# Kernel optimization log

Measured on AMD Instinct MI355X. Metric: run time of the kernel, lower is better.

The kernel has to match this reference:

```python
import jax, jax.numpy as jnp
import numpy as np

N, E, R = 50000, 1600000, 8
IN_F, HID_F, OUT_F = 128, 64, 64


def setup_inputs() -> dict:
    key = jax.random.key(0)
    ks = jax.random.split(key, 9)
    x = jax.random.normal(ks[0], (N, IN_F), dtype=jnp.float32)
    edge_index = jax.random.randint(ks[1], (2, E), 0, N, dtype=jnp.int64)
    edge_type = jax.random.randint(ks[2], (E,), 0, R, dtype=jnp.int64)
    # layer 1 params (scaled like glorot)
    s1 = 1.0 / np.sqrt(IN_F)
    W1_rel = jax.random.normal(ks[3], (R, IN_F, HID_F), dtype=jnp.float32) * s1
    W1_root = jax.random.normal(ks[4], (IN_F, HID_F), dtype=jnp.float32) * s1
    b1 = jnp.zeros((HID_F,), dtype=jnp.float32)
    # layer 2 params
    s2 = 1.0 / np.sqrt(HID_F)
    W2_rel = jax.random.normal(ks[5], (R, HID_F, OUT_F), dtype=jnp.float32) * s2
    W2_root = jax.random.normal(ks[6], (HID_F, OUT_F), dtype=jnp.float32) * s2
    b2 = jnp.zeros((OUT_F,), dtype=jnp.float32)
    return {"x": x, "edge_index": edge_index, "edge_type": edge_type,
            "W1_rel": W1_rel, "W1_root": W1_root, "b1": b1,
            "W2_rel": W2_rel, "W2_root": W2_root, "b2": b2}


def _rgcn_conv(x, src, dst, etype, W_rel, W_root, b):
    """PyG RGCNConv: root transform + per-relation mean-aggregated messages."""
    n = x.shape[0]
    r = W_rel.shape[0]
    # per-relation transform of all node features: [R, N, H]
    xw = jnp.einsum('nd,rdh->rnh', x, W_rel)
    # per-edge message: transformed source feature under the edge's relation
    msg = xw[etype, src]  # [E, H]
    # mean normalization per (dst, relation) pair
    key = dst * r + etype  # [E]
    cnt = jax.ops.segment_sum(jnp.ones(etype.shape, dtype=x.dtype), key,
                              num_segments=n * r)
    inv = 1.0 / jnp.maximum(cnt, 1.0)
    msg = msg * inv[key][:, None]
    # scatter-add into target nodes
    agg = jax.ops.segment_sum(msg, dst, num_segments=n)  # [N, H]
    return agg + x @ W_root + b


def reference(x, edge_index, edge_type, W1_rel, W1_root, b1, W2_rel, W2_root, b2):
    src, dst = edge_index[0], edge_index[1]
    h = _rgcn_conv(x, src, dst, edge_type, W1_rel, W1_root, b1)
    h = jax.nn.relu(h)
    out = _rgcn_conv(h, src, dst, edge_type, W2_rel, W2_root, b2)
    return out
```

## Files before the change

### kernel.cpp

```cpp
#include <hip/hip_runtime.h>


constexpr int NN  = 50000;
constexpr int NE  = 1600000;
constexpr int NR  = 8;
constexpr int FIN = 128;
constexpr int FH  = 64;

constexpr int BSH = 7;
constexpr int BN  = 1 << BSH;
constexpr int NB  = (NN + BN - 1) >> BSH;
constexpr int CAP = 6144;
constexpr int CH  = 4096;
constexpr int NAPP = (NE + CH - 1) / CH;
constexpr unsigned XWMAX = (unsigned)(NN - 1) * (NR * 64) + (NR - 1) * 64;

typedef __attribute__((ext_vector_type(8))) short bf16x8;
typedef __attribute__((ext_vector_type(4))) float f32x4;

__device__ __forceinline__ unsigned short f2bf(float f) {
  unsigned u = __float_as_uint(f);
  u = (u + 0x7fff + ((u >> 16) & 1)) >> 16;
  return (unsigned short)u;
}
__device__ __forceinline__ float bf2f(unsigned short b) {
  return __uint_as_float(((unsigned)b) << 16);
}
__device__ __forceinline__ bool edge_ok(unsigned s, unsigned d, unsigned r) {
  return s < NN && d < NN && r < NR;
}

__device__ void append_body(char* smem, int bx,
                            const int* __restrict__ src,
                            const int* __restrict__ dst,
                            const int* __restrict__ et,
                            int* __restrict__ bcur,
                            unsigned* __restrict__ brecs) {
  uint2* stage = (uint2*)smem;
  int* h     = (int*)(smem + (size_t)CH * 8);
  int* gbase = h + NB;
  int* sbase = gbase + NB;
  int* scur  = sbase + NB;
  int* wtot  = scur + NB;

  const int t  = threadIdx.x;
  const int c0 = bx * CH;
  const int m  = min(CH, NE - c0);

  for (int i = t; i < NB; i += 256) h[i] = 0;
  __syncthreads();

  for (int i = t; i < m; i += 256) {
    const unsigned s = (unsigned)src[c0 + i];
    const unsigned d = (unsigned)dst[c0 + i];
    const unsigned r = (unsigned)et[c0 + i];
    if (edge_ok(s, d, r)) atomicAdd(&h[d >> BSH], 1);
  }
  __syncthreads();

  const int v0 = (2 * t < NB) ? h[2 * t] : 0;
  const int v1 = (2 * t + 1 < NB) ? h[2 * t + 1] : 0;
  if (2 * t < NB     && v0) gbase[2 * t]     = atomicAdd(&bcur[2 * t], v0);
  if (2 * t + 1 < NB && v1) gbase[2 * t + 1] = atomicAdd(&bcur[2 * t + 1], v1);
  const int s = v0 + v1;
  int incl = s;
#pragma unroll
  for (int o = 1; o < 64; o <<= 1) {
    int u = __shfl_up(incl, o, 64);
    if ((t & 63) >= o) incl += u;
  }
  if ((t & 63) == 63) wtot[t >> 6] = incl;
  __syncthreads();
  int wo = 0;
  for (int w = 0; w < (t >> 6); ++w) wo += wtot[w];
  const int e = wo + incl - s;
  if (2 * t < NB)     { sbase[2 * t] = e;          scur[2 * t] = e; }
  if (2 * t + 1 < NB) { sbase[2 * t + 1] = e + v0; scur[2 * t + 1] = e + v0; }
  __syncthreads();

  for (int i = t; i < m; i += 256) {
    const unsigned sv = (unsigned)src[c0 + i];
    const unsigned d  = (unsigned)dst[c0 + i];
    const unsigned r  = (unsigned)et[c0 + i];
    if (edge_ok(sv, d, r)) {
      const int p = atomicAdd(&scur[d >> BSH], 1);
      if (p < CH) stage[p] = make_uint2((sv << 10) | (((unsigned)d & (BN - 1)) << 3) | r, d);
    }
  }
  __syncthreads();

  const int M = min(sbase[NB - 1] + h[NB - 1], CH);
  for (int j = t; j < M; j += 256) {
    const uint2 rec = stage[j];
    const int b = (int)(rec.y >> BSH);
    const int idx = min(gbase[b] + (j - sbase[b]), NB * CAP - 1);
    brecs[idx] = rec.x;
  }
}

__global__ void __launch_bounds__(256) bucket_finalize(
    const int* __restrict__ bcur, const unsigned* __restrict__ brecs,
    int* __restrict__ row_start, int* __restrict__ deg,
    unsigned* __restrict__ recs) {
  const int b    = blockIdx.x;
  const int base = b * CAP;
  const int m    = min(bcur[b] - base, CAP);
  const int d0   = b << BSH;
  __shared__ int cnt[BN * NR];
  __shared__ int curs[BN * NR];
  __shared__ int wtot[4];
  const int t = threadIdx.x;

  for (int i = t; i < BN * NR; i += 256) cnt[i] = 0;
  __syncthreads();
  for (int i = t; i < m; i += 256) {
    const unsigned rec = brecs[base + i];
    const int dl = (int)((rec >> 3) & (BN - 1));
    const int r  = (int)(rec & 7);
    atomicAdd(&cnt[dl * NR + r], 1);
  }
  __syncthreads();

  const int c0 = cnt[t * 4], c1 = cnt[t * 4 + 1], c2 = cnt[t * 4 + 2], c3 = cnt[t * 4 + 3];
  const int s = c0 + c1 + c2 + c3;
  int incl = s;
#pragma unroll
  for (int o = 1; o < 64; o <<= 1) {
    int u = __shfl_up(incl, o, 64);
    if ((t & 63) >= o) incl += u;
  }
  if ((t & 63) == 63) wtot[t >> 6] = incl;
  __syncthreads();
  int wo = 0;
  for (int w = 0; w < (t >> 6); ++w) wo += wtot[w];
  const int e = wo + incl - s;
  curs[t * 4]     = e;
  curs[t * 4 + 1] = e + c0;
  curs[t * 4 + 2] = e + c0 + c1;
  curs[t * 4 + 3] = e + c0 + c1 + c2;
  __syncthreads();

  if (t < BN) {
    const int d = d0 + t;
    if (d < NN) {
      const int start = curs[t * NR];
      const int end   = (t == BN - 1) ? m : curs[(t + 1) * NR];
      row_start[d] = base + start;
      deg[d]       = end - start;
    }
  }
  __syncthreads();

  for (int i = t; i < m; i += 256) {
    const unsigned rec = brecs[base + i];
    const int dl = (int)((rec >> 3) & (BN - 1));
    const int r  = (int)(rec & 7);
    const unsigned sv = rec >> 10;
    const int p  = atomicAdd(&curs[dl * NR + r], 1);
    const unsigned cn = (unsigned)min(cnt[dl * NR + r], 127);
    recs[base + min(p, CAP - 1)] = (cn << 25) | (sv << 9) | ((unsigned)r << 6);
  }
}

__global__ void prep(const float* __restrict__ W1r, const float* __restrict__ W1o,
                     const float* __restrict__ W2r, const float* __restrict__ W2o,
                     unsigned short* __restrict__ Wt1,
                     unsigned short* __restrict__ Wt2,
                     int* __restrict__ bcur) {
  const int i  = blockIdx.x * blockDim.x + threadIdx.x;
  if (i < NB) bcur[i] = i * CAP;
  const int n1 = (NR + 1) * 64 * FIN;
  const int n2 = (NR + 1) * 64 * FH;
  if (i < n1) {
    const int g = i / (64 * FIN), rem = i % (64 * FIN);
    const int n = rem / FIN, k = rem % FIN;
    const float* W = (g < NR) ? (W1r + (size_t)g * FIN * 64) : W1o;
    Wt1[i] = f2bf(W[k * 64 + n]);
  } else if (i < n1 + n2) {
    const int j = i - n1;
    const int g = j / (64 * FH), rem = j % (64 * FH);
    const int n = rem / FH, k = rem % FH;
    const float* W = (g < NR) ? (W2r + (size_t)g * FH * 64) : W2o;
    Wt2[j] = f2bf(W[k * 64 + n]);
  }
}

template <int K, bool A_FP32>
__device__ void gemm_body(char* smem, int bx,
                          const void* __restrict__ Av,
                          const unsigned short* __restrict__ Wt,
                          const float* __restrict__ bias,
                          unsigned short* __restrict__ xw,
                          float* __restrict__ root_out) {
  constexpr int KP  = K + 8;
  constexpr int NCH = 64 * (K / 8) / 256;
  constexpr int NKC = K / 32;
  unsigned short* Bs0 = (unsigned short*)smem;
  const int n0  = bx * 64;
  const int tid = threadIdx.x;
  const int wave = tid >> 6, lane = tid & 63;
  const int i16 = lane & 15, quad = lane >> 4;
  const int r0 = wave * 16 + i16;
  const int arow = n0 + r0;

  bf16x8 afrag[NKC];
  if constexpr (A_FP32) {
    const float* A = (const float*)Av;
#pragma unroll
    for (int kc = 0; kc < NKC; ++kc) {
      bf16x8 v = {};
      if (arow < NN) {
        const float* p = A + (size_t)arow * K + kc * 32 + quad * 8;
        const float4 f0 = *(const float4*)p;
        const float4 f1 = *(const float4*)(p + 4);
        v[0] = f2bf(f0.x); v[1] = f2bf(f0.y); v[2] = f2bf(f0.z); v[3] = f2bf(f0.w);
        v[4] = f2bf(f1.x); v[5] = f2bf(f1.y); v[6] = f2bf(f1.z); v[7] = f2bf(f1.w);
      }
      afrag[kc] = v;
    }
  } else {
    const unsigned short* A = (const unsigned short*)Av;
#pragma unroll
    for (int kc = 0; kc < NKC; ++kc) {
      bf16x8 v = {};
      if (arow < NN) v = *(const bf16x8*)(A + (size_t)arow * K + kc * 32 + quad * 8);
      afrag[kc] = v;
    }
  }

  for (int c = 0; c < NCH; ++c) {
    const int idx = tid + c * 256;
    const int row = idx / (K / 8), kp = (idx % (K / 8)) * 8;
    *(bf16x8*)(Bs0 + row * KP + kp) = *(const bf16x8*)(Wt + idx * 8);
  }
  __syncthreads();

  for (int g = 0; g <= NR; ++g) {
    const int buf = g & 1;
    unsigned short* Bc = Bs0 + buf * 64 * KP;
    unsigned short* Bn = Bs0 + (buf ^ 1) * 64 * KP;
    bf16x8 breg[NCH];
    if (g < NR) {
      const unsigned short* Wn = Wt + (size_t)(g + 1) * 64 * K;
#pragma unroll
      for (int c = 0; c < NCH; ++c) breg[c] = *(const bf16x8*)(Wn + (tid + c * 256) * 8);
    }

    f32x4 acc[4] = {};
#pragma unroll
    for (int kc = 0; kc < NKC; ++kc) {
      const int k0 = kc * 32 + quad * 8;
      const bf16x8 a0 = afrag[kc];
      const bf16x8 b0 = *(const bf16x8*)(Bc + (i16)      * KP + k0);
      const bf16x8 b1 = *(const bf16x8*)(Bc + (i16 + 16) * KP + k0);
      const bf16x8 b2 = *(const bf16x8*)(Bc + (i16 + 32) * KP + k0);
      const bf16x8 b3 = *(const bf16x8*)(Bc + (i16 + 48) * KP + k0);
      acc[0] = __builtin_amdgcn_mfma_f32_16x16x32_bf16(a0, b0, acc[0], 0, 0, 0);
      acc[1] = __builtin_amdgcn_mfma_f32_16x16x32_bf16(a0, b1, acc[1], 0, 0, 0);
      acc[2] = __builtin_amdgcn_mfma_f32_16x16x32_bf16(a0, b2, acc[2], 0, 0, 0);
      acc[3] = __builtin_amdgcn_mfma_f32_16x16x32_bf16(a0, b3, acc[3], 0, 0, 0);
    }

    if (g < NR) {
#pragma unroll
      for (int c = 0; c < NCH; ++c) {
        const int idx = tid + c * 256;
        const int row = idx / (K / 8), kp = (idx % (K / 8)) * 8;
        *(bf16x8*)(Bn + row * KP + kp) = breg[c];
      }
#pragma unroll
      for (int reg = 0; reg < 4; ++reg) {
        const int n = n0 + wave * 16 + quad * 4 + reg;
        if (n >= NN) continue;
        unsigned short* p = xw + (size_t)n * (NR * 64) + g * 64 + i16;
#pragma unroll
        for (int ct = 0; ct < 4; ++ct) p[ct * 16] = f2bf(acc[ct][reg]);
      }
    } else {
      float bv[4];
#pragma unroll
      for (int ct = 0; ct < 4; ++ct) bv[ct] = bias[ct * 16 + i16];
#pragma unroll
      for (int reg = 0; reg < 4; ++reg) {
        const int n = n0 + wave * 16 + quad * 4 + reg;
        if (n >= NN) continue;
        float* p = root_out + (size_t)n * 64 + i16;
#pragma unroll
        for (int ct = 0; ct < 4; ++ct) p[ct * 16] = acc[ct][reg] + bv[ct];
      }
    }
    __syncthreads();
  }
}

__global__ void __launch_bounds__(256) fused_append_gemm1(
    const int* __restrict__ src, const int* __restrict__ dst,
    const int* __restrict__ et, int* __restrict__ bcur,
    unsigned* __restrict__ brecs,
    const float* __restrict__ A, const unsigned short* __restrict__ Wt,
    const float* __restrict__ bias, unsigned short* __restrict__ xw,
    float* __restrict__ root_out) {
  extern __shared__ char smem[];
  const int bx = (int)blockIdx.x;
  if (bx % 3 == 2 && bx / 3 < NAPP)
    append_body(smem, bx / 3, src, dst, et, bcur, brecs);
  else
    gemm_body<FIN, true>(smem, bx - (bx + 1) / 3, A, Wt, bias, xw, root_out);
}

__global__ void __launch_bounds__(256) gemm_l2(
    const unsigned short* __restrict__ A, const unsigned short* __restrict__ Wt,
    const float* __restrict__ bias, unsigned short* __restrict__ xw,
    float* __restrict__ out) {
  extern __shared__ char smem[];
  gemm_body<FH, false>(smem, (int)blockIdx.x, A, Wt, bias, xw, out);
}

template <bool RELU_BF16>
__global__ void __launch_bounds__(256) agg_csr(
    const int* __restrict__ row_start, const int* __restrict__ deg,
    const unsigned* __restrict__ recs, const unsigned short* __restrict__ xw,
    const float* __restrict__ root,
    float* __restrict__ out_f32, unsigned short* __restrict__ out_b16) {
  const int gid  = blockIdx.x * blockDim.x + threadIdx.x;
  const int lane = gid & 63;
  const int wv   = gid >> 6;
  const int half = lane >> 5;
  const int sub  = lane & 31;
  const int e  = sub >> 3;
  const int l8 = sub & 7;
  const int d  = wv * 2 + half;
  if (d >= NN) return;
  const int base = row_start[d];
  const int n    = deg[d];
  const unsigned* po = recs + base;
  const unsigned short* xp = xw + l8 * 8;
  float a[8] = {};

  for (int i0 = 0; i0 < n; i0 += 32) {
    unsigned rr[8];
#pragma unroll
    for (int sl = 0; sl < 8; ++sl) {
      const int i = i0 + e + 4 * sl;
      rr[sl] = (i < n) ? po[i] : 0u;
    }
    bf16x8 vv[8];
#pragma unroll
    for (int sl = 0; sl < 8; ++sl) {
      const unsigned u = min(rr[sl] & 0x01FFFFFFu, XWMAX);
      vv[sl] = *(const bf16x8*)(xp + u);
    }
#pragma unroll
    for (int sl = 0; sl < 8; ++sl) {
      float w = __builtin_amdgcn_rcpf((float)(rr[sl] >> 25));
      if (i0 + e + 4 * sl >= n) w = 0.f;
#pragma unroll
      for (int q = 0; q < 8; ++q) a[q] += bf2f((unsigned short)vv[sl][q]) * w;
    }
  }

#pragma unroll
  for (int q = 0; q < 8; ++q) {
    a[q] += __shfl_xor(a[q], 8, 64);
    a[q] += __shfl_xor(a[q], 16, 64);
  }

  if (e == 0) {
    const float4 r0 = *(const float4*)(root + (size_t)d * 64 + l8 * 8);
    const float4 r1 = *(const float4*)(root + (size_t)d * 64 + l8 * 8 + 4);
    const float o[8] = {r0.x + a[0], r0.y + a[1], r0.z + a[2], r0.w + a[3],
                        r1.x + a[4], r1.y + a[5], r1.z + a[6], r1.w + a[7]};
    if (RELU_BF16) {
      bf16x8 ov;
#pragma unroll
      for (int q = 0; q < 8; ++q) ov[q] = (short)f2bf(fmaxf(o[q], 0.f));
      *(bf16x8*)(out_b16 + (size_t)d * 64 + l8 * 8) = ov;
    } else {
      *(float4*)(out_f32 + (size_t)d * 64 + l8 * 8)     = make_float4(o[0], o[1], o[2], o[3]);
      *(float4*)(out_f32 + (size_t)d * 64 + l8 * 8 + 4) = make_float4(o[4], o[5], o[6], o[7]);
    }
  }
}

extern "C" void kernel_launch(void* const* d_in, const int* in_sizes, int n_in,
                              void* d_out, int out_size, void* d_ws, size_t ws_size,
                              hipStream_t stream) {
  const float* x   = (const float*)d_in[0];
  const int*   ei  = (const int*)d_in[1];
  const int*   et  = (const int*)d_in[2];
  const float* W1r = (const float*)d_in[3];
  const float* W1o = (const float*)d_in[4];
  const float* b1  = (const float*)d_in[5];
  const float* W2r = (const float*)d_in[6];
  const float* W2o = (const float*)d_in[7];
  const float* b2  = (const float*)d_in[8];
  float* out = (float*)d_out;

  const int* src = ei;
  const int* dst = ei + NE;

  char* ws = (char*)d_ws;
  size_t off = 0;
  auto alloc = [&](size_t bytes) {
    void* p = ws + off; off += (bytes + 255) & ~(size_t)255; return p;
  };
  int*   bcur      = (int*)alloc((size_t)NB * 4);
  int*   row_start = (int*)alloc((size_t)NN * 4);
  int*   deg       = (int*)alloc((size_t)NN * 4);
  unsigned* brecs  = (unsigned*)alloc((size_t)NB * CAP * 4);
  unsigned* offs   = (unsigned*)alloc((size_t)NB * CAP * 4);
  unsigned short* xw    = (unsigned short*)alloc((size_t)NN * NR * 64 * 2);
  unsigned short* hb    = (unsigned short*)alloc((size_t)NN * FH * 2);
  float*          hroot = (float*)alloc((size_t)NN * 64 * 4);
  unsigned short* Wt1   = (unsigned short*)alloc((size_t)(NR + 1) * 64 * FIN * 2);
  unsigned short* Wt2   = (unsigned short*)alloc((size_t)(NR + 1) * 64 * FH * 2);

  const int nprep = (NR + 1) * 64 * (FIN + FH);
  prep<<<(nprep + 255) / 256, 256, 0, stream>>>(W1r, W1o, W2r, W2o, Wt1, Wt2, bcur);

  const int gemm_blocks = (NN + 63) / 64;
  const int agg_blocks  = ((NN + 1) / 2 + 3) / 4;
  constexpr int SM1 = CH * 8 + 4 * NB * 4 + 16;
  constexpr int SM2 = 2 * 64 * (FH + 8) * 2;

  fused_append_gemm1<<<NAPP + gemm_blocks, 256, SM1, stream>>>(
      src, dst, et, bcur, brecs, x, Wt1, b1, xw, hroot);
  bucket_finalize<<<NB, 256, 0, stream>>>(bcur, brecs, row_start, deg, offs);

  agg_csr<true><<<agg_blocks, 256, 0, stream>>>(row_start, deg, offs, xw, hroot, nullptr, hb);
  gemm_l2<<<gemm_blocks, 256, SM2, stream>>>(hb, Wt2, b2, xw, out);
  agg_csr<false><<<agg_blocks, 256, 0, stream>>>(row_start, deg, offs, xw, out, out, nullptr);
}
```

Measured before the change: 244.1 us.

## Reorder layer-2 as aggregate-then-transform with a single concatenated-K GEMM

```diff
diff --git a/kernel.cpp b/kernel.cpp
--- a/kernel.cpp
+++ b/kernel.cpp
@@ -14,6 +14,8 @@
 constexpr int CH  = 4096;
 constexpr int NAPP = (NE + CH - 1) / CH;
 constexpr unsigned XWMAX = (unsigned)(NN - 1) * (NR * 64) + (NR - 1) * 64;
+constexpr int K2  = 576;
+constexpr int K2P = 584;
 
 typedef __attribute__((ext_vector_type(8))) short bf16x8;
 typedef __attribute__((ext_vector_type(4))) float f32x4;
@@ -101,7 +103,7 @@
 __global__ void __launch_bounds__(256) bucket_finalize(
     const int* __restrict__ bcur, const unsigned* __restrict__ brecs,
     int* __restrict__ row_start, int* __restrict__ deg,
-    unsigned* __restrict__ recs) {
+    unsigned* __restrict__ recs, unsigned* __restrict__ segs) {
   const int b    = blockIdx.x;
   const int base = b * CAP;
   const int m    = min(bcur[b] - base, CAP);
@@ -147,6 +149,12 @@
       const int end   = (t == BN - 1) ? m : curs[(t + 1) * NR];
       row_start[d] = base + start;
       deg[d]       = end - start;
+#pragma unroll
+      for (int r = 0; r < NR; ++r) {
+        const unsigned st = (unsigned)(base + curs[t * NR + r]);
+        const unsigned cn = (unsigned)min(cnt[t * NR + r], 255);
+        segs[(size_t)d * NR + r] = (st << 8) | cn;
+      }
     }
   }
   __syncthreads();
@@ -165,12 +173,12 @@
 __global__ void prep(const float* __restrict__ W1r, const float* __restrict__ W1o,
                      const float* __restrict__ W2r, const float* __restrict__ W2o,
                      unsigned short* __restrict__ Wt1,
-                     unsigned short* __restrict__ Wt2,
+                     unsigned short* __restrict__ Wt2b,
                      int* __restrict__ bcur) {
   const int i  = blockIdx.x * blockDim.x + threadIdx.x;
   if (i < NB) bcur[i] = i * CAP;
   const int n1 = (NR + 1) * 64 * FIN;
-  const int n2 = (NR + 1) * 64 * FH;
+  const int n2 = 64 * K2;
   if (i < n1) {
     const int g = i / (64 * FIN), rem = i % (64 * FIN);
     const int n = rem / FIN, k = rem % FIN;
@@ -178,10 +186,16 @@
     Wt1[i] = f2bf(W[k * 64 + n]);
   } else if (i < n1 + n2) {
     const int j = i - n1;
-    const int g = j / (64 * FH), rem = j % (64 * FH);
-    const int n = rem / FH, k = rem % FH;
-    const float* W = (g < NR) ? (W2r + (size_t)g * FH * 64) : W2o;
-    Wt2[j] = f2bf(W[k * 64 + n]);
+    const int n = j / K2, c = j % K2;
+    float v;
+    if (c < 512) {
+      const int r = c >> 6, kk = c & 63;
+      v = W2r[((size_t)r * 64 + kk) * 64 + n];
+    } else {
+      const int kk = c - 512;
+      v = W2o[(size_t)kk * 64 + n];
+    }
+    Wt2b[j] = f2bf(v);
   }
 }
 
@@ -308,40 +322,28 @@
     gemm_body<FIN, true>(smem, bx - (bx + 1) / 3, A, Wt, bias, xw, root_out);
 }
 
-__global__ void __launch_bounds__(256) gemm_l2(
-    const unsigned short* __restrict__ A, const unsigned short* __restrict__ Wt,
-    const float* __restrict__ bias, unsigned short* __restrict__ xw,
-    float* __restrict__ out) {
-  extern __shared__ char smem[];
-  gemm_body<FH, false>(smem, (int)blockIdx.x, A, Wt, bias, xw, out);
-}
-
-template <bool RELU_BF16>
-__global__ void __launch_bounds__(256) agg_csr(
+__global__ void __launch_bounds__(256) agg1(
     const int* __restrict__ row_start, const int* __restrict__ deg,
     const unsigned* __restrict__ recs, const unsigned short* __restrict__ xw,
-    const float* __restrict__ root,
-    float* __restrict__ out_f32, unsigned short* __restrict__ out_b16) {
+    const float* __restrict__ root, unsigned short* __restrict__ out_b16) {
   const int gid  = blockIdx.x * blockDim.x + threadIdx.x;
   const int lane = gid & 63;
-  const int wv   = gid >> 6;
-  const int half = lane >> 5;
-  const int sub  = lane & 31;
-  const int e  = sub >> 3;
-  const int l8 = sub & 7;
-  const int d  = wv * 2 + half;
+  const int d    = gid >> 6;
   if (d >= NN) return;
+  const int e  = lane >> 3;
+  const int l8 = lane & 7;
   const int base = row_start[d];
   const int n    = deg[d];
   const unsigned* po = recs + base;
   const unsigned short* xp = xw + l8 * 8;
   float a[8] = {};
 
-  for (int i0 = 0; i0 < n; i0 += 32) {
+  int i0 = 0;
+  for (; i0 + 32 < n; i0 += 64) {
     unsigned rr[8];
 #pragma unroll
     for (int sl = 0; sl < 8; ++sl) {
-      const int i = i0 + e + 4 * sl;
+      const int i = i0 + e + 8 * sl;
       rr[sl] = (i < n) ? po[i] : 0u;
     }
     bf16x8 vv[8];
@@ -353,7 +355,28 @@
 #pragma unroll
     for (int sl = 0; sl < 8; ++sl) {
       float w = __builtin_amdgcn_rcpf((float)(rr[sl] >> 25));
-      if (i0 + e + 4 * sl >= n) w = 0.f;
+      if (i0 + e + 8 * sl >= n) w = 0.f;
+#pragma unroll
+      for (int q = 0; q < 8; ++q) a[q] += bf2f((unsigned short)vv[sl][q]) * w;
+    }
+  }
+  if (i0 < n) {
+    unsigned rr[4];
+#pragma unroll
+    for (int sl = 0; sl < 4; ++sl) {
+      const int i = i0 + e + 8 * sl;
+      rr[sl] = (i < n) ? po[i] : 0u;
+    }
+    bf16x8 vv[4];
+#pragma unroll
+    for (int sl = 0; sl < 4; ++sl) {
+      const unsigned u = min(rr[sl] & 0x01FFFFFFu, XWMAX);
+      vv[sl] = *(const bf16x8*)(xp + u);
+    }
+#pragma unroll
+    for (int sl = 0; sl < 4; ++sl) {
+      float w = __builtin_amdgcn_rcpf((float)(rr[sl] >> 25));
+      if (i0 + e + 8 * sl >= n) w = 0.f;
 #pragma unroll
       for (int q = 0; q < 8; ++q) a[q] += bf2f((unsigned short)vv[sl][q]) * w;
     }
@@ -363,6 +386,7 @@
   for (int q = 0; q < 8; ++q) {
     a[q] += __shfl_xor(a[q], 8, 64);
     a[q] += __shfl_xor(a[q], 16, 64);
+    a[q] += __shfl_xor(a[q], 32, 64);
   }
 
   if (e == 0) {
@@ -370,14 +394,109 @@
     const float4 r1 = *(const float4*)(root + (size_t)d * 64 + l8 * 8 + 4);
     const float o[8] = {r0.x + a[0], r0.y + a[1], r0.z + a[2], r0.w + a[3],
                         r1.x + a[4], r1.y + a[5], r1.z + a[6], r1.w + a[7]};
-    if (RELU_BF16) {
-      bf16x8 ov;
-#pragma unroll
-      for (int q = 0; q < 8; ++q) ov[q] = (short)f2bf(fmaxf(o[q], 0.f));
-      *(bf16x8*)(out_b16 + (size_t)d * 64 + l8 * 8) = ov;
-    } else {
-      *(float4*)(out_f32 + (size_t)d * 64 + l8 * 8)     = make_float4(o[0], o[1], o[2], o[3]);
-      *(float4*)(out_f32 + (size_t)d * 64 + l8 * 8 + 4) = make_float4(o[4], o[5], o[6], o[7]);
+    bf16x8 ov;
+#pragma unroll
+    for (int q = 0; q < 8; ++q) ov[q] = (short)f2bf(fmaxf(o[q], 0.f));
+    *(bf16x8*)(out_b16 + (size_t)d * 64 + l8 * 8) = ov;
+  }
+}
+
+__global__ void __launch_bounds__(256) agg2_sums(
+    const unsigned* __restrict__ segs, const unsigned* __restrict__ recs,
+    const unsigned short* __restrict__ hb, unsigned short* __restrict__ sums) {
+  const int gid  = blockIdx.x * blockDim.x + threadIdx.x;
+  const int lane = gid & 63;
+  const int d    = gid >> 6;
+  if (d >= NN) return;
+  const int r  = lane >> 3;
+  const int l8 = lane & 7;
+  const unsigned sg = segs[(size_t)d * NR + r];
+  const int start = (int)(sg >> 8);
+  const int len   = (int)(sg & 255u);
+  const unsigned* po = recs + start;
+  const unsigned short* hp = hb + l8 * 8;
+  float a[8] = {};
+
+  for (int j = 0; j < len; j += 4) {
+    unsigned rr[4];
+#pragma unroll
+    for (int sl = 0; sl < 4; ++sl)
+      rr[sl] = (j + sl < len) ? po[j + sl] : 0u;
+    bf16x8 vv[4];
+#pragma unroll
+    for (int sl = 0; sl < 4; ++sl) {
+      const unsigned sv = (rr[sl] >> 9) & 0xFFFFu;
+      vv[sl] = *(const bf16x8*)(hp + sv * 64);
+    }
+#pragma unroll
+    for (int sl = 0; sl < 4; ++sl) {
+      const float wk = (j + sl < len) ? 1.f : 0.f;
+#pragma unroll
+      for (int q = 0; q < 8; ++q) a[q] += bf2f((unsigned short)vv[sl][q]) * wk;
+    }
+  }
+
+  const float w = (len > 0) ? __builtin_amdgcn_rcpf((float)len) : 0.f;
+  bf16x8 ov;
+#pragma unroll
+  for (int q = 0; q < 8; ++q) ov[q] = (short)f2bf(a[q] * w);
+  *(bf16x8*)(sums + (size_t)d * K2 + r * 64 + l8 * 8) = ov;
+
+  if (lane < 8) {
+    const bf16x8 hv = *(const bf16x8*)(hb + (size_t)d * 64 + lane * 8);
+    *(bf16x8*)(sums + (size_t)d * K2 + 512 + lane * 8) = hv;
+  }
+}
+
+__global__ void __launch_bounds__(256) gemm_final(
+    const unsigned short* __restrict__ A,
+    const unsigned short* __restrict__ Wt,
+    const float* __restrict__ bias, float* __restrict__ out) {
+  __shared__ unsigned short Bs[64 * K2P];
+  const int tid = threadIdx.x;
+  const int wave = tid >> 6, lane = tid & 63;
+  const int i16 = lane & 15, quad = lane >> 4;
+  const int n0 = (int)blockIdx.x * 64;
+  const int node = n0 + wave * 16 + i16;
+
+#pragma unroll
+  for (int c = 0; c < 18; ++c) {
+    const int idx = tid + c * 256;
+    const int row = idx / 72, kp = (idx % 72) * 8;
+    *(bf16x8*)(Bs + row * K2P + kp) = *(const bf16x8*)(Wt + idx * 8);
+  }
+
+  bf16x8 afrag[18];
+#pragma unroll
+  for (int kc = 0; kc < 18; ++kc) {
+    bf16x8 v = {};
+    if (node < NN) v = *(const bf16x8*)(A + (size_t)node * K2 + kc * 32 + quad * 8);
+    afrag[kc] = v;
+  }
+  __syncthreads();
+
+  f32x4 acc[4] = {};
+#pragma unroll
+  for (int kc = 0; kc < 18; ++kc) {
+    const int k0 = kc * 32 + quad * 8;
+    const bf16x8 a0 = afrag[kc];
+    const bf16x8 b0 = *(const bf16x8*)(Bs + (i16)      * K2P + k0);
+    const bf16x8 b1 = *(const bf16x8*)(Bs + (i16 + 16) * K2P + k0);
+    const bf16x8 b2 = *(const bf16x8*)(Bs + (i16 + 32) * K2P + k0);
+    const bf16x8 b3 = *(const bf16x8*)(Bs + (i16 + 48) * K2P + k0);
+    acc[0] = __builtin_amdgcn_mfma_f32_16x16x32_bf16(b0, a0, acc[0], 0, 0, 0);
+    acc[1] = __builtin_amdgcn_mfma_f32_16x16x32_bf16(b1, a0, acc[1], 0, 0, 0);
+    acc[2] = __builtin_amdgcn_mfma_f32_16x16x32_bf16(b2, a0, acc[2], 0, 0, 0);
+    acc[3] = __builtin_amdgcn_mfma_f32_16x16x32_bf16(b3, a0, acc[3], 0, 0, 0);
+  }
+
+  if (node < NN) {
+#pragma unroll
+    for (int ct = 0; ct < 4; ++ct) {
+      const float4 bv = *(const float4*)(bias + ct * 16 + quad * 4);
+      float* p = out + (size_t)node * 64 + ct * 16 + quad * 4;
+      *(float4*)p = make_float4(acc[ct][0] + bv.x, acc[ct][1] + bv.y,
+                                acc[ct][2] + bv.z, acc[ct][3] + bv.w);
     }
   }
 }
@@ -407,27 +526,28 @@
   int*   bcur      = (int*)alloc((size_t)NB * 4);
   int*   row_start = (int*)alloc((size_t)NN * 4);
   int*   deg       = (int*)alloc((size_t)NN * 4);
+  unsigned* segs   = (unsigned*)alloc((size_t)NN * NR * 4);
   unsigned* brecs  = (unsigned*)alloc((size_t)NB * CAP * 4);
-  unsigned* offs   = (unsigned*)alloc((size_t)NB * CAP * 4);
+  unsigned* recs   = (unsigned*)alloc((size_t)NB * CAP * 4);
   unsigned short* xw    = (unsigned short*)alloc((size_t)NN * NR * 64 * 2);
   unsigned short* hb    = (unsigned short*)alloc((size_t)NN * FH * 2);
   float*          hroot = (float*)alloc((size_t)NN * 64 * 4);
+  unsigned short* sums  = (unsigned short*)alloc((size_t)NN * K2 * 2);
   unsigned short* Wt1   = (unsigned short*)alloc((size_t)(NR + 1) * 64 * FIN * 2);
-  unsigned short* Wt2   = (unsigned short*)alloc((size_t)(NR + 1) * 64 * FH * 2);
-
-  const int nprep = (NR + 1) * 64 * (FIN + FH);
-  prep<<<(nprep + 255) / 256, 256, 0, stream>>>(W1r, W1o, W2r, W2o, Wt1, Wt2, bcur);
+  unsigned short* Wt2b  = (unsigned short*)alloc((size_t)64 * K2 * 2);
+
+  const int nprep = (NR + 1) * 64 * FIN + 64 * K2;
+  prep<<<(nprep + 255) / 256, 256, 0, stream>>>(W1r, W1o, W2r, W2o, Wt1, Wt2b, bcur);
 
   const int gemm_blocks = (NN + 63) / 64;
-  const int agg_blocks  = ((NN + 1) / 2 + 3) / 4;
+  const int agg_blocks  = (NN * 64 + 255) / 256;
   constexpr int SM1 = CH * 8 + 4 * NB * 4 + 16;
-  constexpr int SM2 = 2 * 64 * (FH + 8) * 2;
 
   fused_append_gemm1<<<NAPP + gemm_blocks, 256, SM1, stream>>>(
       src, dst, et, bcur, brecs, x, Wt1, b1, xw, hroot);
-  bucket_finalize<<<NB, 256, 0, stream>>>(bcur, brecs, row_start, deg, offs);
-
-  agg_csr<true><<<agg_blocks, 256, 0, stream>>>(row_start, deg, offs, xw, hroot, nullptr, hb);
-  gemm_l2<<<gemm_blocks, 256, SM2, stream>>>(hb, Wt2, b2, xw, out);
-  agg_csr<false><<<agg_blocks, 256, 0, stream>>>(row_start, deg, offs, xw, out, out, nullptr);
-}
+  bucket_finalize<<<NB, 256, 0, stream>>>(bcur, brecs, row_start, deg, recs, segs);
+
+  agg1<<<agg_blocks, 256, 0, stream>>>(row_start, deg, recs, xw, hroot, hb);
+  agg2_sums<<<agg_blocks, 256, 0, stream>>>(segs, recs, hb, sums);
+  gemm_final<<<gemm_blocks, 256, 0, stream>>>(sums, Wt2b, b2, out);
+}
```

New measurement: 242.5 us. Within noise of the previous version (-0.7%).
